# Kernel tuning notes

Hardware: AMD Instinct MI355X
Metric: run time of the kernel (lower is better)

## Reference

```python
import jax, jax.numpy as jnp
import numpy as np

P = 512       # protein_dim
D = 512       # drug_dim
N = 2000      # neighbors per layer
E = 300000    # binding edges per layer
ND = 100000   # total drugs
BASELINE = 6.0
LN_EPS = 1e-5


def setup_inputs() -> dict:
    key = jax.random.key(0)
    ks = jax.random.split(key, 24)
    inp = {
        "target_features": jax.random.normal(ks[0], (P,), jnp.float32),
        "form_features": jax.random.normal(ks[1], (N, P), jnp.float32),
        "role_features": jax.random.normal(ks[2], (N, P), jnp.float32),
        "form_neighbors": jnp.arange(N, dtype=jnp.int64) if jax.config.jax_enable_x64 else jnp.arange(N, dtype=jnp.int32),
        "role_neighbors": jnp.arange(N, dtype=jnp.int32),
        "form_binds_ei": jax.random.randint(ks[3], (2, E), 0, N, jnp.int32),
        "form_binds_y": jax.random.uniform(ks[4], (E,), jnp.float32) * 8.0 + 2.0,
        "role_binds_ei": jax.random.randint(ks[5], (2, E), 0, N, jnp.int32),
        "role_binds_y": jax.random.uniform(ks[6], (E,), jnp.float32) * 8.0 + 2.0,
        "drug_features": jax.random.normal(ks[7], (ND, D), jnp.float32),
    }
    inp["form_neighbors"] = jnp.arange(N, dtype=jnp.int32)
    attn_in = P * 2 + 16
    s1 = 1.0 / np.sqrt(attn_in)
    s2 = 1.0 / np.sqrt(64)
    sd = 1.0 / np.sqrt(D)
    sp = 1.0 / np.sqrt(P)
    inp["layer_emb"] = jax.random.normal(ks[8], (2, 16), jnp.float32)
    inp["W1"] = jax.random.uniform(ks[9], (attn_in, 64), jnp.float32, -s1, s1)
    inp["b1"] = jax.random.uniform(ks[10], (64,), jnp.float32, -s1, s1)
    inp["W2"] = jax.random.uniform(ks[11], (64, 1), jnp.float32, -s2, s2)
    inp["b2"] = jax.random.uniform(ks[12], (1,), jnp.float32, -s2, s2)
    inp["Wi1"] = jax.random.uniform(ks[13], (D, P), jnp.float32, -sd, sd)
    inp["bi1"] = jax.random.uniform(ks[14], (P,), jnp.float32, -sd, sd)
    inp["prelu_alpha"] = jnp.array(0.25, jnp.float32)
    inp["Wi2"] = jax.random.uniform(ks[15], (P, P), jnp.float32, -sp, sp)
    inp["bi2"] = jax.random.uniform(ks[16], (P,), jnp.float32, -sp, sp)
    inp["ln_gamma"] = jnp.ones((P,), jnp.float32)
    inp["ln_beta"] = jnp.zeros((P,), jnp.float32)
    return inp


def _pref_vectors(neighbor_ids, ei, y, drug_features):
    # Vectorized form of the per-neighbor masked gather-sum:
    # for each edge, find its neighbor slot (neighbor_ids is sorted);
    # edges whose src id is not a neighbor get zero weight.
    n = neighbor_ids.shape[0]
    pos = jnp.clip(jnp.searchsorted(neighbor_ids, ei[0]), 0, n - 1)
    valid = neighbor_ids[pos] == ei[0]
    w = jnp.where(valid, y - BASELINE, 0.0)              # [E]
    contrib = drug_features[ei[1]] * w[:, None]          # [E, D] gather (memory-bound)
    return jax.ops.segment_sum(contrib, pos, num_segments=n)  # [N, D]


def _attention(z_target, z_neighbors, l_vec, W1, b1, W2, b2):
    n = z_neighbors.shape[0]
    inp = jnp.concatenate(
        [jnp.broadcast_to(z_target, (n, z_target.shape[0])),
         z_neighbors,
         jnp.broadcast_to(l_vec, (n, l_vec.shape[0]))], axis=-1)  # [N, 2P+16]
    h = inp @ W1 + b1
    h = jnp.where(h > 0, h, 0.2 * h)  # LeakyReLU(0.2)
    return h @ W2 + b2                # [N, 1]


def reference(target_features, form_features, role_features, form_neighbors,
              role_neighbors, form_binds_ei, form_binds_y, role_binds_ei,
              role_binds_y, drug_features, layer_emb, W1, b1, W2, b2,
              Wi1, bi1, prelu_alpha, Wi2, bi2, ln_gamma, ln_beta):
    form_msgs = _pref_vectors(form_neighbors, form_binds_ei, form_binds_y, drug_features)
    role_msgs = _pref_vectors(role_neighbors, role_binds_ei, role_binds_y, drug_features)

    form_attn = _attention(target_features, form_features, layer_emb[0], W1, b1, W2, b2)
    role_attn = _attention(target_features, role_features, layer_emb[1], W1, b1, W2, b2)

    all_msgs = jnp.concatenate([form_msgs, role_msgs], axis=0)   # [2N, D]
    all_attn = jnp.concatenate([form_attn, role_attn], axis=0)   # [2N, 1]
    attn_weights = jax.nn.softmax(all_attn, axis=0)
    v_prior = jnp.sum(attn_weights * all_msgs, axis=0)           # [D]

    h = v_prior @ Wi1 + bi1
    h = jnp.where(h > 0, h, prelu_alpha * h)  # PReLU
    v = h @ Wi2 + bi2                          # [P]

    x = target_features + v
    mu = jnp.mean(x)
    var = jnp.mean(jnp.square(x - mu))
    z_refined = (x - mu) / jnp.sqrt(var + LN_EPS) * ln_gamma + ln_beta
    return (z_refined, form_msgs, role_msgs)
```

## Files before the change

### kernel.cpp

```cpp
#include <hip/hip_runtime.h>
#include <math.h>

static constexpr int PD = 512;
static constexpr float BASEV = 6.0f;
static constexpr int CAP = 320;

__global__ void edge_kernel(const int* __restrict__ ei_f, const float* __restrict__ y_f,
                            const int* __restrict__ ei_r, const float* __restrict__ y_r,
                            const int* __restrict__ nb_f, const int* __restrict__ nb_r,
                            int N, int E, int* __restrict__ cnt,
                            int* __restrict__ sj, float* __restrict__ sw) {
    int i = blockIdx.x * blockDim.x + threadIdx.x;
    if (i >= 2 * E) return;
    bool role = i >= E;
    int e = role ? i - E : i;
    const int* ei0 = role ? ei_r : ei_f;
    const int* ei1 = (role ? ei_r : ei_f) + E;
    int v = ei0[e];
    const int* nb = role ? nb_r : nb_f;
    int lo = 0, hi = N;
    while (lo < hi) { int mid = (lo + hi) >> 1; if (nb[mid] < v) lo = mid + 1; else hi = mid; }
    int pos = lo < N ? lo : N - 1;
    if (nb[pos] != v) return;
    int s = role ? N + pos : pos;
    int j = ei1[e];
    float w = (role ? y_r[e] : y_f[e]) - BASEV;
    int slot = atomicAdd(&cnt[s], 1);
    if (slot < CAP) { sj[s * CAP + slot] = j; sw[s * CAP + slot] = w; }
}

__global__ __launch_bounds__(128) void accum_kernel(const int* __restrict__ cnt,
                                                    const int* __restrict__ sj,
                                                    const float* __restrict__ sw,
                                                    const float* __restrict__ drug,
                                                    float* __restrict__ msgs) {
    int b = blockIdx.x;
    int t = threadIdx.x;
    int n = cnt[b]; n = n < CAP ? n : CAP;
    const int* sjb = sj + b * CAP;
    const float* swb = sw + b * CAP;
    float4 acc = make_float4(0.f, 0.f, 0.f, 0.f);
    int k = 0;
    for (; k + 3 < n; k += 4) {
        int j0 = sjb[k], j1 = sjb[k + 1], j2 = sjb[k + 2], j3 = sjb[k + 3];
        float w0 = swb[k], w1 = swb[k + 1], w2 = swb[k + 2], w3 = swb[k + 3];
        float4 d0 = ((const float4*)(drug + (size_t)j0 * PD))[t];
        float4 d1 = ((const float4*)(drug + (size_t)j1 * PD))[t];
        float4 d2 = ((const float4*)(drug + (size_t)j2 * PD))[t];
        float4 d3 = ((const float4*)(drug + (size_t)j3 * PD))[t];
        acc.x += w0 * d0.x; acc.y += w0 * d0.y; acc.z += w0 * d0.z; acc.w += w0 * d0.w;
        acc.x += w1 * d1.x; acc.y += w1 * d1.y; acc.z += w1 * d1.z; acc.w += w1 * d1.w;
        acc.x += w2 * d2.x; acc.y += w2 * d2.y; acc.z += w2 * d2.z; acc.w += w2 * d2.w;
        acc.x += w3 * d3.x; acc.y += w3 * d3.y; acc.z += w3 * d3.z; acc.w += w3 * d3.w;
    }
    for (; k < n; k++) {
        int j0 = sjb[k];
        float w0 = swb[k];
        float4 d0 = ((const float4*)(drug + (size_t)j0 * PD))[t];
        acc.x += w0 * d0.x; acc.y += w0 * d0.y; acc.z += w0 * d0.z; acc.w += w0 * d0.w;
    }
    ((float4*)(msgs + (size_t)b * PD))[t] = acc;
}

__global__ void attn_const_kernel(const float* __restrict__ target, const float* __restrict__ lemb,
                                  const float* __restrict__ W1, const float* __restrict__ b1,
                                  float* __restrict__ cbuf) {
    int l = blockIdx.x, j = threadIdx.x;
    float c = b1[j];
    for (int p = 0; p < PD; p++) c += target[p] * W1[p * 64 + j];
    for (int q = 0; q < 16; q++) c += lemb[l * 16 + q] * W1[(2 * PD + q) * 64 + j];
    cbuf[l * 64 + j] = c;
}

__global__ __launch_bounds__(256) void attn_kernel(const float* __restrict__ formF,
                                                   const float* __restrict__ roleF,
                                                   const float* __restrict__ W1,
                                                   const float* __restrict__ W2,
                                                   const float* __restrict__ b2,
                                                   const float* __restrict__ cbuf,
                                                   int N, float* __restrict__ logits) {
    int wave = threadIdx.x >> 6, lane = threadIdx.x & 63;
    int s = blockIdx.x * 4 + wave;
    if (s >= 2 * N) return;
    int rl = s >= N ? 1 : 0;
    const float* z = rl ? roleF + (size_t)(s - N) * PD : formF + (size_t)s * PD;
    const float* w1p = W1 + PD * 64 + lane;
    float h0 = cbuf[rl * 64 + lane], h1 = 0.f, h2 = 0.f, h3 = 0.f;
    for (int p = 0; p < PD; p += 4) {
        h0 += z[p + 0] * w1p[(size_t)(p + 0) * 64];
        h1 += z[p + 1] * w1p[(size_t)(p + 1) * 64];
        h2 += z[p + 2] * w1p[(size_t)(p + 2) * 64];
        h3 += z[p + 3] * w1p[(size_t)(p + 3) * 64];
    }
    float h = (h0 + h1) + (h2 + h3);
    h = h > 0.f ? h : 0.2f * h;
    float v = h * W2[lane];
#pragma unroll
    for (int off = 32; off > 0; off >>= 1) v += __shfl_down(v, off, 64);
    if (lane == 0) logits[s] = v + b2[0];
}

__global__ __launch_bounds__(128) void vprior_kernel(const float* __restrict__ logits,
                                                     const float* __restrict__ msgs,
                                                     int nseg, float* __restrict__ v_prior) {
    __shared__ float red[128];
    int t = threadIdx.x;
    float m = -1e30f;
    for (int s = t; s < nseg; s += 128) m = fmaxf(m, logits[s]);
    red[t] = m; __syncthreads();
    for (int o = 64; o > 0; o >>= 1) { if (t < o) red[t] = fmaxf(red[t], red[t + o]); __syncthreads(); }
    m = red[0]; __syncthreads();
    float sum = 0.f;
    for (int s = t; s < nseg; s += 128) sum += expf(logits[s] - m);
    red[t] = sum; __syncthreads();
    for (int o = 64; o > 0; o >>= 1) { if (t < o) red[t] += red[t + o]; __syncthreads(); }
    float inv = 1.f / red[0];

    float4 acc = make_float4(0.f, 0.f, 0.f, 0.f);
    for (int s = blockIdx.x; s < nseg; s += gridDim.x) {
        float w = expf(logits[s] - m) * inv;
        float4 d = ((const float4*)(msgs + (size_t)s * PD))[t];
        acc.x += w * d.x; acc.y += w * d.y; acc.z += w * d.z; acc.w += w * d.w;
    }
    atomicAdd(&v_prior[4 * t + 0], acc.x);
    atomicAdd(&v_prior[4 * t + 1], acc.y);
    atomicAdd(&v_prior[4 * t + 2], acc.z);
    atomicAdd(&v_prior[4 * t + 3], acc.w);
}

__global__ __launch_bounds__(256) void mv1_kernel(const float* __restrict__ v_prior,
                                                  const float* __restrict__ Wi1,
                                                  float* __restrict__ h) {
    int b = blockIdx.x;
    int t = threadIdx.x;
    float2 acc = make_float2(0.f, 0.f);
    int d0 = b * 16;
    for (int d = d0; d < d0 + 16; d++) {
        float vd = v_prior[d];
        float2 w = ((const float2*)(Wi1 + (size_t)d * PD))[t];
        acc.x += vd * w.x; acc.y += vd * w.y;
    }
    atomicAdd(&h[2 * t + 0], acc.x);
    atomicAdd(&h[2 * t + 1], acc.y);
}

__global__ __launch_bounds__(256) void mv2_kernel(const float* __restrict__ h,
                                                  const float* __restrict__ bi1,
                                                  const float* __restrict__ alpha_p,
                                                  const float* __restrict__ Wi2,
                                                  float* __restrict__ v) {
    int b = blockIdx.x;
    int t = threadIdx.x;
    float alpha = alpha_p[0];
    float2 acc = make_float2(0.f, 0.f);
    int q0 = b * 16;
    for (int q = q0; q < q0 + 16; q++) {
        float hq = h[q] + bi1[q];
        hq = hq > 0.f ? hq : alpha * hq;
        float2 w = ((const float2*)(Wi2 + (size_t)q * PD))[t];
        acc.x += hq * w.x; acc.y += hq * w.y;
    }
    atomicAdd(&v[2 * t + 0], acc.x);
    atomicAdd(&v[2 * t + 1], acc.y);
}

__global__ __launch_bounds__(512) void final_kernel(const float* __restrict__ target,
                                                    const float* __restrict__ v,
                                                    const float* __restrict__ bi2,
                                                    const float* __restrict__ gamma,
                                                    const float* __restrict__ beta,
                                                    float* __restrict__ out) {
    __shared__ float red[512];
    int t = threadIdx.x;
    float x = target[t] + v[t] + bi2[t];
    red[t] = x; __syncthreads();
    for (int o = 256; o > 0; o >>= 1) { if (t < o) red[t] += red[t + o]; __syncthreads(); }
    float mu = red[0] * (1.f / 512.f);
    __syncthreads();
    float dx = x - mu;
    red[t] = dx * dx; __syncthreads();
    for (int o = 256; o > 0; o >>= 1) { if (t < o) red[t] += red[t + o]; __syncthreads(); }
    float var = red[0] * (1.f / 512.f);
    out[t] = dx * (1.f / sqrtf(var + 1e-5f)) * gamma[t] + beta[t];
}

extern "C" void kernel_launch(void* const* d_in, const int* in_sizes, int n_in,
                              void* d_out, int out_size, void* d_ws, size_t ws_size,
                              hipStream_t stream) {
    const float* target = (const float*)d_in[0];
    const float* formF  = (const float*)d_in[1];
    const float* roleF  = (const float*)d_in[2];
    const int*   nb_f   = (const int*)d_in[3];
    const int*   nb_r   = (const int*)d_in[4];
    const int*   ei_f   = (const int*)d_in[5];
    const float* y_f    = (const float*)d_in[6];
    const int*   ei_r   = (const int*)d_in[7];
    const float* y_r    = (const float*)d_in[8];
    const float* drug   = (const float*)d_in[9];
    const float* lemb   = (const float*)d_in[10];
    const float* W1     = (const float*)d_in[11];
    const float* b1     = (const float*)d_in[12];
    const float* W2     = (const float*)d_in[13];
    const float* b2     = (const float*)d_in[14];
    const float* Wi1    = (const float*)d_in[15];
    const float* bi1    = (const float*)d_in[16];
    const float* alpha  = (const float*)d_in[17];
    const float* Wi2    = (const float*)d_in[18];
    const float* bi2    = (const float*)d_in[19];
    const float* gamma  = (const float*)d_in[20];
    const float* beta   = (const float*)d_in[21];

    int N = in_sizes[3];
    int E = in_sizes[5] / 2;
    int nseg = 2 * N;

    int* ws = (int*)d_ws;
    int*   cnt     = ws + 0;
    float* v_prior = (float*)(ws + 4096);
    float* hbuf    = (float*)(ws + 4608);
    float* vbuf    = (float*)(ws + 5120);
    float* cbuf    = (float*)(ws + 5632);
    float* logits  = (float*)(ws + 5760);
    int*   sj      = ws + 9856;
    float* sw      = (float*)(sj + 4096 * CAP);

    float* out  = (float*)d_out;
    float* msgs = out + PD;

    hipMemsetAsync(ws, 0, 5632 * sizeof(int), stream);

    int nb2E = (2 * E + 255) / 256;
    edge_kernel<<<nb2E, 256, 0, stream>>>(ei_f, y_f, ei_r, y_r, nb_f, nb_r, N, E, cnt, sj, sw);
    attn_const_kernel<<<2, 64, 0, stream>>>(target, lemb, W1, b1, cbuf);
    attn_kernel<<<(nseg + 3) / 4, 256, 0, stream>>>(formF, roleF, W1, W2, b2, cbuf, N, logits);
    accum_kernel<<<nseg, 128, 0, stream>>>(cnt, sj, sw, drug, msgs);
    vprior_kernel<<<64, 128, 0, stream>>>(logits, msgs, nseg, v_prior);
    mv1_kernel<<<32, 256, 0, stream>>>(v_prior, Wi1, hbuf);
    mv2_kernel<<<32, 256, 0, stream>>>(hbuf, bi1, alpha, Wi2, vbuf);
    final_kernel<<<1, 512, 0, stream>>>(target, vbuf, bi2, gamma, beta, out);
}
```

Measured before the change: 501.5 us.

## Fuse launches: merged attention/edge kernel, packed bins, single tail kernel

```diff
diff --git a/kernel.cpp b/kernel.cpp
--- a/kernel.cpp
+++ b/kernel.cpp
@@ -5,104 +5,116 @@
 static constexpr float BASEV = 6.0f;
 static constexpr int CAP = 320;
 
-__global__ void edge_kernel(const int* __restrict__ ei_f, const float* __restrict__ y_f,
-                            const int* __restrict__ ei_r, const float* __restrict__ y_r,
-                            const int* __restrict__ nb_f, const int* __restrict__ nb_r,
-                            int N, int E, int* __restrict__ cnt,
-                            int* __restrict__ sj, float* __restrict__ sw) {
-    int i = blockIdx.x * blockDim.x + threadIdx.x;
-    if (i >= 2 * E) return;
-    bool role = i >= E;
-    int e = role ? i - E : i;
-    const int* ei0 = role ? ei_r : ei_f;
-    const int* ei1 = (role ? ei_r : ei_f) + E;
-    int v = ei0[e];
-    const int* nb = role ? nb_r : nb_f;
-    int lo = 0, hi = N;
-    while (lo < hi) { int mid = (lo + hi) >> 1; if (nb[mid] < v) lo = mid + 1; else hi = mid; }
-    int pos = lo < N ? lo : N - 1;
-    if (nb[pos] != v) return;
-    int s = role ? N + pos : pos;
-    int j = ei1[e];
-    float w = (role ? y_r[e] : y_f[e]) - BASEV;
-    int slot = atomicAdd(&cnt[s], 1);
-    if (slot < CAP) { sj[s * CAP + slot] = j; sw[s * CAP + slot] = w; }
+static constexpr int OFF_CNT    = 0;
+static constexpr int OFF_CBUF   = 4096;
+static constexpr int OFF_LOGITS = 4224;
+static constexpr int OFF_VPART  = 8320;
+static constexpr int OFF_BINS   = 41088;
+
+__global__ void init_kernel(const float* __restrict__ target, const float* __restrict__ lemb,
+                            const float* __restrict__ W1, const float* __restrict__ b1,
+                            int* __restrict__ cnt, float* __restrict__ cbuf) {
+    int t = threadIdx.x;
+    if (blockIdx.x == 0) {
+#pragma unroll
+        for (int k = 0; k < 16; k++) cnt[k * 256 + t] = 0;
+    } else if (t < 128) {
+        int l = t >> 6, j = t & 63;
+        float c = b1[j];
+        for (int p = 0; p < PD; p++) c += target[p] * W1[p * 64 + j];
+        for (int q = 0; q < 16; q++) c += lemb[l * 16 + q] * W1[(2 * PD + q) * 64 + j];
+        cbuf[l * 64 + j] = c;
+    }
+}
+
+__global__ __launch_bounds__(256) void work_kernel(
+        const int* __restrict__ ei_f, const float* __restrict__ y_f,
+        const int* __restrict__ ei_r, const float* __restrict__ y_r,
+        const int* __restrict__ nb_f, const int* __restrict__ nb_r,
+        const float* __restrict__ formF, const float* __restrict__ roleF,
+        const float* __restrict__ W1, const float* __restrict__ W2,
+        const float* __restrict__ b2, const float* __restrict__ cbuf,
+        int N, int E, int nAttn,
+        int* __restrict__ cnt, int2* __restrict__ bins, float* __restrict__ logits) {
+    if (blockIdx.x < (unsigned)nAttn) {
+        int wave = threadIdx.x >> 6, lane = threadIdx.x & 63;
+        int s = blockIdx.x * 4 + wave;
+        if (s >= 2 * N) return;
+        int rl = s >= N ? 1 : 0;
+        const float* z = rl ? roleF + (size_t)(s - N) * PD : formF + (size_t)s * PD;
+        const float4* z4 = (const float4*)z;
+        const float* w1p = W1 + PD * 64 + lane;
+        float h0 = cbuf[rl * 64 + lane], h1 = 0.f, h2 = 0.f, h3 = 0.f;
+        for (int p = 0; p < PD; p += 4) {
+            float4 zv = z4[p >> 2];
+            h0 += zv.x * w1p[(size_t)(p + 0) * 64];
+            h1 += zv.y * w1p[(size_t)(p + 1) * 64];
+            h2 += zv.z * w1p[(size_t)(p + 2) * 64];
+            h3 += zv.w * w1p[(size_t)(p + 3) * 64];
+        }
+        float h = (h0 + h1) + (h2 + h3);
+        h = h > 0.f ? h : 0.2f * h;
+        float v = h * W2[lane];
+#pragma unroll
+        for (int off = 32; off > 0; off >>= 1) v += __shfl_down(v, off, 64);
+        if (lane == 0) logits[s] = v + b2[0];
+    } else {
+        int i = (blockIdx.x - nAttn) * blockDim.x + threadIdx.x;
+        if (i >= 2 * E) return;
+        bool role = i >= E;
+        int e = role ? i - E : i;
+        const int* ei0 = role ? ei_r : ei_f;
+        const int* ei1 = (role ? ei_r : ei_f) + E;
+        int v = ei0[e];
+        const int* nb = role ? nb_r : nb_f;
+        int lo = 0, hi = N;
+        while (lo < hi) { int mid = (lo + hi) >> 1; if (nb[mid] < v) lo = mid + 1; else hi = mid; }
+        int pos = lo < N ? lo : N - 1;
+        if (nb[pos] != v) return;
+        int s = role ? N + pos : pos;
+        float w = (role ? y_r[e] : y_f[e]) - BASEV;
+        int slot = atomicAdd(&cnt[s], 1);
+        if (slot < CAP) bins[s * CAP + slot] = make_int2(ei1[e], __float_as_int(w));
+    }
 }
 
 __global__ __launch_bounds__(128) void accum_kernel(const int* __restrict__ cnt,
-                                                    const int* __restrict__ sj,
-                                                    const float* __restrict__ sw,
+                                                    const int2* __restrict__ bins,
                                                     const float* __restrict__ drug,
                                                     float* __restrict__ msgs) {
+    __shared__ int2 lbin[CAP];
     int b = blockIdx.x;
     int t = threadIdx.x;
     int n = cnt[b]; n = n < CAP ? n : CAP;
-    const int* sjb = sj + b * CAP;
-    const float* swb = sw + b * CAP;
+    for (int k = t; k < n; k += 128) lbin[k] = bins[b * CAP + k];
+    __syncthreads();
     float4 acc = make_float4(0.f, 0.f, 0.f, 0.f);
     int k = 0;
     for (; k + 3 < n; k += 4) {
-        int j0 = sjb[k], j1 = sjb[k + 1], j2 = sjb[k + 2], j3 = sjb[k + 3];
-        float w0 = swb[k], w1 = swb[k + 1], w2 = swb[k + 2], w3 = swb[k + 3];
-        float4 d0 = ((const float4*)(drug + (size_t)j0 * PD))[t];
-        float4 d1 = ((const float4*)(drug + (size_t)j1 * PD))[t];
-        float4 d2 = ((const float4*)(drug + (size_t)j2 * PD))[t];
-        float4 d3 = ((const float4*)(drug + (size_t)j3 * PD))[t];
+        int2 e0 = lbin[k], e1 = lbin[k + 1], e2 = lbin[k + 2], e3 = lbin[k + 3];
+        float4 d0 = ((const float4*)(drug + (size_t)e0.x * PD))[t];
+        float4 d1 = ((const float4*)(drug + (size_t)e1.x * PD))[t];
+        float4 d2 = ((const float4*)(drug + (size_t)e2.x * PD))[t];
+        float4 d3 = ((const float4*)(drug + (size_t)e3.x * PD))[t];
+        float w0 = __int_as_float(e0.y), w1 = __int_as_float(e1.y);
+        float w2 = __int_as_float(e2.y), w3 = __int_as_float(e3.y);
         acc.x += w0 * d0.x; acc.y += w0 * d0.y; acc.z += w0 * d0.z; acc.w += w0 * d0.w;
         acc.x += w1 * d1.x; acc.y += w1 * d1.y; acc.z += w1 * d1.z; acc.w += w1 * d1.w;
         acc.x += w2 * d2.x; acc.y += w2 * d2.y; acc.z += w2 * d2.z; acc.w += w2 * d2.w;
         acc.x += w3 * d3.x; acc.y += w3 * d3.y; acc.z += w3 * d3.z; acc.w += w3 * d3.w;
     }
     for (; k < n; k++) {
-        int j0 = sjb[k];
-        float w0 = swb[k];
-        float4 d0 = ((const float4*)(drug + (size_t)j0 * PD))[t];
+        int2 e0 = lbin[k];
+        float w0 = __int_as_float(e0.y);
+        float4 d0 = ((const float4*)(drug + (size_t)e0.x * PD))[t];
         acc.x += w0 * d0.x; acc.y += w0 * d0.y; acc.z += w0 * d0.z; acc.w += w0 * d0.w;
     }
     ((float4*)(msgs + (size_t)b * PD))[t] = acc;
-}
-
-__global__ void attn_const_kernel(const float* __restrict__ target, const float* __restrict__ lemb,
-                                  const float* __restrict__ W1, const float* __restrict__ b1,
-                                  float* __restrict__ cbuf) {
-    int l = blockIdx.x, j = threadIdx.x;
-    float c = b1[j];
-    for (int p = 0; p < PD; p++) c += target[p] * W1[p * 64 + j];
-    for (int q = 0; q < 16; q++) c += lemb[l * 16 + q] * W1[(2 * PD + q) * 64 + j];
-    cbuf[l * 64 + j] = c;
-}
-
-__global__ __launch_bounds__(256) void attn_kernel(const float* __restrict__ formF,
-                                                   const float* __restrict__ roleF,
-                                                   const float* __restrict__ W1,
-                                                   const float* __restrict__ W2,
-                                                   const float* __restrict__ b2,
-                                                   const float* __restrict__ cbuf,
-                                                   int N, float* __restrict__ logits) {
-    int wave = threadIdx.x >> 6, lane = threadIdx.x & 63;
-    int s = blockIdx.x * 4 + wave;
-    if (s >= 2 * N) return;
-    int rl = s >= N ? 1 : 0;
-    const float* z = rl ? roleF + (size_t)(s - N) * PD : formF + (size_t)s * PD;
-    const float* w1p = W1 + PD * 64 + lane;
-    float h0 = cbuf[rl * 64 + lane], h1 = 0.f, h2 = 0.f, h3 = 0.f;
-    for (int p = 0; p < PD; p += 4) {
-        h0 += z[p + 0] * w1p[(size_t)(p + 0) * 64];
-        h1 += z[p + 1] * w1p[(size_t)(p + 1) * 64];
-        h2 += z[p + 2] * w1p[(size_t)(p + 2) * 64];
-        h3 += z[p + 3] * w1p[(size_t)(p + 3) * 64];
-    }
-    float h = (h0 + h1) + (h2 + h3);
-    h = h > 0.f ? h : 0.2f * h;
-    float v = h * W2[lane];
-#pragma unroll
-    for (int off = 32; off > 0; off >>= 1) v += __shfl_down(v, off, 64);
-    if (lane == 0) logits[s] = v + b2[0];
 }
 
 __global__ __launch_bounds__(128) void vprior_kernel(const float* __restrict__ logits,
                                                      const float* __restrict__ msgs,
-                                                     int nseg, float* __restrict__ v_prior) {
+                                                     int nseg, float* __restrict__ v_part) {
     __shared__ float red[128];
     int t = threadIdx.x;
     float m = -1e30f;
@@ -122,57 +134,48 @@
         float4 d = ((const float4*)(msgs + (size_t)s * PD))[t];
         acc.x += w * d.x; acc.y += w * d.y; acc.z += w * d.z; acc.w += w * d.w;
     }
-    atomicAdd(&v_prior[4 * t + 0], acc.x);
-    atomicAdd(&v_prior[4 * t + 1], acc.y);
-    atomicAdd(&v_prior[4 * t + 2], acc.z);
-    atomicAdd(&v_prior[4 * t + 3], acc.w);
-}
-
-__global__ __launch_bounds__(256) void mv1_kernel(const float* __restrict__ v_prior,
-                                                  const float* __restrict__ Wi1,
-                                                  float* __restrict__ h) {
-    int b = blockIdx.x;
-    int t = threadIdx.x;
-    float2 acc = make_float2(0.f, 0.f);
-    int d0 = b * 16;
-    for (int d = d0; d < d0 + 16; d++) {
-        float vd = v_prior[d];
-        float2 w = ((const float2*)(Wi1 + (size_t)d * PD))[t];
-        acc.x += vd * w.x; acc.y += vd * w.y;
-    }
-    atomicAdd(&h[2 * t + 0], acc.x);
-    atomicAdd(&h[2 * t + 1], acc.y);
-}
-
-__global__ __launch_bounds__(256) void mv2_kernel(const float* __restrict__ h,
-                                                  const float* __restrict__ bi1,
-                                                  const float* __restrict__ alpha_p,
-                                                  const float* __restrict__ Wi2,
-                                                  float* __restrict__ v) {
-    int b = blockIdx.x;
-    int t = threadIdx.x;
+    ((float4*)(v_part + (size_t)blockIdx.x * PD))[t] = acc;
+}
+
+__global__ __launch_bounds__(512) void tail_kernel(const float* __restrict__ v_part,
+                                                   const float* __restrict__ Wi1,
+                                                   const float* __restrict__ bi1,
+                                                   const float* __restrict__ alpha_p,
+                                                   const float* __restrict__ Wi2,
+                                                   const float* __restrict__ bi2,
+                                                   const float* __restrict__ target,
+                                                   const float* __restrict__ gamma,
+                                                   const float* __restrict__ beta,
+                                                   float* __restrict__ out) {
+    __shared__ float vp[512];
+    __shared__ float hs[512];
+    __shared__ float red[512];
+    int t = threadIdx.x;
+    float a = 0.f;
+#pragma unroll
+    for (int i = 0; i < 64; i++) a += v_part[i * PD + t];
+    vp[t] = a;
+    __syncthreads();
+
+    float h = bi1[t];
+    for (int d = 0; d < PD; d += 4) {
+        h += vp[d + 0] * Wi1[(size_t)(d + 0) * PD + t];
+        h += vp[d + 1] * Wi1[(size_t)(d + 1) * PD + t];
+        h += vp[d + 2] * Wi1[(size_t)(d + 2) * PD + t];
+        h += vp[d + 3] * Wi1[(size_t)(d + 3) * PD + t];
+    }
     float alpha = alpha_p[0];
-    float2 acc = make_float2(0.f, 0.f);
-    int q0 = b * 16;
-    for (int q = q0; q < q0 + 16; q++) {
-        float hq = h[q] + bi1[q];
-        hq = hq > 0.f ? hq : alpha * hq;
-        float2 w = ((const float2*)(Wi2 + (size_t)q * PD))[t];
-        acc.x += hq * w.x; acc.y += hq * w.y;
-    }
-    atomicAdd(&v[2 * t + 0], acc.x);
-    atomicAdd(&v[2 * t + 1], acc.y);
-}
-
-__global__ __launch_bounds__(512) void final_kernel(const float* __restrict__ target,
-                                                    const float* __restrict__ v,
-                                                    const float* __restrict__ bi2,
-                                                    const float* __restrict__ gamma,
-                                                    const float* __restrict__ beta,
-                                                    float* __restrict__ out) {
-    __shared__ float red[512];
-    int t = threadIdx.x;
-    float x = target[t] + v[t] + bi2[t];
+    hs[t] = h > 0.f ? h : alpha * h;
+    __syncthreads();
+
+    float v = bi2[t];
+    for (int q = 0; q < PD; q += 4) {
+        v += hs[q + 0] * Wi2[(size_t)(q + 0) * PD + t];
+        v += hs[q + 1] * Wi2[(size_t)(q + 1) * PD + t];
+        v += hs[q + 2] * Wi2[(size_t)(q + 2) * PD + t];
+        v += hs[q + 3] * Wi2[(size_t)(q + 3) * PD + t];
+    }
+    float x = target[t] + v;
     red[t] = x; __syncthreads();
     for (int o = 256; o > 0; o >>= 1) { if (t < o) red[t] += red[t + o]; __syncthreads(); }
     float mu = red[0] * (1.f / 512.f);
@@ -215,27 +218,24 @@
     int nseg = 2 * N;
 
     int* ws = (int*)d_ws;
-    int*   cnt     = ws + 0;
-    float* v_prior = (float*)(ws + 4096);
-    float* hbuf    = (float*)(ws + 4608);
-    float* vbuf    = (float*)(ws + 5120);
-    float* cbuf    = (float*)(ws + 5632);
-    float* logits  = (float*)(ws + 5760);
-    int*   sj      = ws + 9856;
-    float* sw      = (float*)(sj + 4096 * CAP);
+    int*   cnt     = ws + OFF_CNT;
+    float* cbuf    = (float*)(ws + OFF_CBUF);
+    float* logits  = (float*)(ws + OFF_LOGITS);
+    float* v_part  = (float*)(ws + OFF_VPART);
+    int2*  bins    = (int2*)(ws + OFF_BINS);
 
     float* out  = (float*)d_out;
     float* msgs = out + PD;
 
-    hipMemsetAsync(ws, 0, 5632 * sizeof(int), stream);
-
-    int nb2E = (2 * E + 255) / 256;
-    edge_kernel<<<nb2E, 256, 0, stream>>>(ei_f, y_f, ei_r, y_r, nb_f, nb_r, N, E, cnt, sj, sw);
-    attn_const_kernel<<<2, 64, 0, stream>>>(target, lemb, W1, b1, cbuf);
-    attn_kernel<<<(nseg + 3) / 4, 256, 0, stream>>>(formF, roleF, W1, W2, b2, cbuf, N, logits);
-    accum_kernel<<<nseg, 128, 0, stream>>>(cnt, sj, sw, drug, msgs);
-    vprior_kernel<<<64, 128, 0, stream>>>(logits, msgs, nseg, v_prior);
-    mv1_kernel<<<32, 256, 0, stream>>>(v_prior, Wi1, hbuf);
-    mv2_kernel<<<32, 256, 0, stream>>>(hbuf, bi1, alpha, Wi2, vbuf);
-    final_kernel<<<1, 512, 0, stream>>>(target, vbuf, bi2, gamma, beta, out);
-}
+    int nAttn = (nseg + 3) / 4;
+    int nEdge = (2 * E + 255) / 256;
+
+    init_kernel<<<2, 256, 0, stream>>>(target, lemb, W1, b1, cnt, cbuf);
+    work_kernel<<<nAttn + nEdge, 256, 0, stream>>>(ei_f, y_f, ei_r, y_r, nb_f, nb_r,
+                                                   formF, roleF, W1, W2, b2, cbuf,
+                                                   N, E, nAttn, cnt, bins, logits);
+    accum_kernel<<<nseg, 128, 0, stream>>>(cnt, bins, drug, msgs);
+    vprior_kernel<<<64, 128, 0, stream>>>(logits, msgs, nseg, v_part);
+    tail_kernel<<<1, 512, 0, stream>>>(v_part, Wi1, bi1, alpha, Wi2, bi2,
+                                       target, gamma, beta, out);
+}
```

New measurement: 514.6 us. 2.6% more time.
